# Kernel tuning notes

Hardware: AMD Instinct MI355X
Metric: run time of the kernel (lower is better)

Reference implementation:

```python
import jax, jax.numpy as jnp
import numpy as np

N = 80000          # nodes
E = 1280000        # edges (~avg degree 16)
D_IN = 64          # Lorentz ambient dim (1 time + 63 spatial feature dims)
D_HID = 64
EPS = 1e-8


def _lorentz_inner(x):
    # <x,x>_L = -x0^2 + ||x_space||^2  (keepdims)
    return -x[:, :1] * x[:, :1] + jnp.sum(x[:, 1:] * x[:, 1:], axis=-1, keepdims=True)


def _to_manifold(s):
    # scale so that <s,s>_L = -1 (curvature c=1 hyperboloid)
    denom = jnp.sqrt(jnp.clip(jnp.abs(_lorentz_inner(s)), EPS))
    return s / denom


def _lorentz_linear(x, W, b, log_scale, nonlin=None):
    # HyboNet LorentzLinear: dense map, then rebuild a valid hyperboloid point
    if nonlin is not None:
        x = nonlin(x)
    h = x @ W.T + b
    time = jax.nn.sigmoid(h[:, :1]) * jnp.exp(log_scale) + 1.1
    space = h[:, 1:]
    sq = jnp.clip(jnp.sum(space * space, axis=-1, keepdims=True), EPS)
    scale = (time * time - 1.0) / sq
    return jnp.concatenate([time, space * jnp.sqrt(scale)], axis=-1)


def _agg(h, src, dst, w):
    # sparse adjacency aggregation (spmm) + Lorentz centroid normalization
    s = jax.ops.segment_sum(w[:, None] * h[src], dst, num_segments=N)
    return _to_manifold(s)


def setup_inputs() -> dict:
    key = jax.random.key(0)
    ks = jax.random.split(key, 6)
    x = jax.random.normal(ks[0], (N, D_IN - 1), jnp.float32)
    edge_index = jax.random.randint(ks[1], (2, E), 0, N, dtype=jnp.int32)
    edge_weight = jax.random.uniform(ks[2], (E,), jnp.float32)
    W1 = jax.random.normal(ks[3], (D_HID, D_IN), jnp.float32) * 0.02
    b1 = jnp.zeros((D_HID,), jnp.float32)
    s1 = jnp.asarray(np.log(10.0), jnp.float32)   # LorentzLinear scale param (log-space)
    W2 = jax.random.normal(ks[4], (D_HID, D_HID), jnp.float32) * 0.02
    b2 = jnp.zeros((D_HID,), jnp.float32)
    s2 = jnp.asarray(np.log(10.0), jnp.float32)
    return dict(x=x, edge_index=edge_index, edge_weight=edge_weight,
                W1=W1, b1=b1, s1=s1, W2=W2, b2=b2, s2=s2)


def reference(x, edge_index, edge_weight, W1, b1, s1, W2, b2, s2):
    src, dst = edge_index[0], edge_index[1]
    n = x.shape[0]
    # lift to Lorentz tangent space at origin: prepend zero time coord
    # (proj_tan0 is then a no-op since time component is already 0)
    u_space = x                                             # [N, D_IN-1]
    # expmap0 (c=1): [cosh(||u||), sinh(||u||) * u/||u||]
    nrm = jnp.clip(jnp.linalg.norm(u_space, axis=-1, keepdims=True), EPS)
    p_space = jnp.sinh(nrm) * u_space / nrm
    # projx: recompute time coord from spatial part, x0 = sqrt(1 + ||x_s||^2)
    p_time = jnp.sqrt(1.0 + jnp.sum(p_space * p_space, axis=-1, keepdims=True))
    p = jnp.concatenate([p_time, p_space], axis=1)          # [N, D_IN]
    # conv1 (no nonlin) and conv2 (relu) = LorentzLinear + Lorentz aggregation
    h1 = _agg(_lorentz_linear(p, W1, b1, s1), src, dst, edge_weight)
    h2 = _agg(_lorentz_linear(h1, W2, b2, s2, nonlin=jax.nn.relu), src, dst, edge_weight)
    # LResNet hyperbolic residual: Lorentz-normalized sum of the two points
    return _to_manifold(h1 + h2)
```

## Files before the change

### kernel.cpp

```cpp
#include <hip/hip_runtime.h>
#include <hip/hip_bf16.h>

#define D 64
#define EPS 1e-8f
#define BSH 8
#define BNODES (1 << BSH)
#define ABLK 8192
#define AUNR 32

typedef __attribute__((ext_vector_type(8))) short bf16x8;
typedef __attribute__((ext_vector_type(4))) float f32x4;
typedef unsigned long long ull;

__device__ __forceinline__ unsigned short f2bf_rn(float f) {
    unsigned u = __float_as_uint(f);
    return (unsigned short)((u + 0x7FFFu + ((u >> 16) & 1u)) >> 16);
}

__device__ __forceinline__ void split8(float4 a, float4 b, bf16x8& h, bf16x8& l) {
    float f[8] = {a.x, a.y, a.z, a.w, b.x, b.y, b.z, b.w};
    #pragma unroll
    for (int i = 0; i < 8; ++i) {
        unsigned u = __float_as_uint(f[i]);
        float hf = __uint_as_float(u & 0xFFFF0000u);
        unsigned lu = __float_as_uint(f[i] - hf);
        h[i] = (short)(u >> 16);
        l[i] = (short)(lu >> 16);
    }
}


__device__ __forceinline__ void embed_body(int bid, const float* __restrict__ x,
                                           float* __restrict__ P, int n) {
    int lane = threadIdx.x & 63, wv = threadIdx.x >> 6;
    int q = lane >> 4, sub = lane & 15;
    int node = bid * 16 + wv * 4 + q;
    if (node >= n) return;
    const float* xr = x + (size_t)node * 63;
    float v0 = 0.f, v1, v2, v3;
    if (sub == 0) {
        v1 = xr[0]; v2 = xr[1]; v3 = xr[2];
    } else {
        int b = sub * 4 - 1;
        v0 = xr[b]; v1 = xr[b + 1]; v2 = xr[b + 2]; v3 = xr[b + 3];
    }
    float s = v0 * v0 + v1 * v1 + v2 * v2 + v3 * v3;
    #pragma unroll
    for (int d2 = 1; d2 < 16; d2 <<= 1) s += __shfl_xor(s, d2);
    float nrm = fmaxf(sqrtf(s), EPS);
    float sh = sinhf(nrm);
    float k = sh / nrm;
    float4 r;
    if (sub == 0) r = make_float4(sqrtf(1.f + sh * sh), k * v1, k * v2, k * v3);
    else          r = make_float4(k * v0, k * v1, k * v2, k * v3);
    *(float4*)(P + (size_t)node * 64 + sub * 4) = r;
}

__device__ __forceinline__ void bcount_body(int bid, const int* __restrict__ dst,
                                            int* __restrict__ bcnt, int e, int nbuck) {
    __shared__ int cnt[320];
    int tid = threadIdx.x;
    for (int b = tid; b < nbuck; b += 256) cnt[b] = 0;
    __syncthreads();
    int i0 = bid * 1024 + tid;
    #pragma unroll
    for (int u = 0; u < 4; ++u) {
        int i = i0 + u * 256;
        if (i < e) atomicAdd(&cnt[dst[i] >> BSH], 1);
    }
    __syncthreads();
    for (int b = tid; b < nbuck; b += 256)
        if (cnt[b]) atomicAdd(&bcnt[b], cnt[b]);
}

__device__ __forceinline__ void bucketA_body(int bid, const int* __restrict__ src,
                                             const int* __restrict__ dst,
                                             const float* __restrict__ w,
                                             int* __restrict__ gcur,
                                             ull* __restrict__ tmp,
                                             int e, int nbuck) {
    __shared__ int cnt[320];
    __shared__ int base[320];
    int tid = threadIdx.x;
    for (int b = tid; b < nbuck; b += 256) cnt[b] = 0;
    __syncthreads();
    int i0 = bid * ABLK + tid;
    int bkt[AUNR], rnk[AUNR];
    #pragma unroll
    for (int u = 0; u < AUNR; ++u) {
        int i = i0 + u * 256;
        if (i < e) {
            int b = dst[i] >> BSH;
            bkt[u] = b;
            rnk[u] = atomicAdd(&cnt[b], 1);
        }
    }
    __syncthreads();
    for (int b = tid; b < nbuck; b += 256) {
        int c = cnt[b];
        base[b] = c ? atomicAdd(&gcur[b], c) : 0;
    }
    __syncthreads();
    #pragma unroll
    for (int u = 0; u < AUNR; ++u) {
        int i = i0 + u * 256;
        if (i < e) {
            ull pk = ((ull)__float_as_uint(w[i]) << 32)
                   | (unsigned)(src[i] | ((dst[i] & (BNODES - 1)) << 20));
            tmp[base[bkt[u]] + rnk[u]] = pk;
        }
    }
}

template <int RELU>
__device__ __forceinline__ void lin_body(int bid, const float* __restrict__ tbl,
                                         const float* __restrict__ W,
                                         const float* __restrict__ bias,
                                         const float* __restrict__ sc,
                                         unsigned short* __restrict__ out, int n) {
    int lane = threadIdx.x & 63, wv = threadIdx.x >> 6;
    int col = lane & 15, grp = lane >> 4;
    int node0 = bid * 64 + wv * 16;
    if (node0 >= n) return;

    float es = expf(sc[0]);

    bf16x8 wh[2][4], wl[2][4];
    #pragma unroll
    for (int s = 0; s < 2; ++s)
        #pragma unroll
        for (int t = 0; t < 4; ++t) {
            const float* wp = W + (t * 16 + col) * 64 + s * 32 + grp * 8;
            split8(*(const float4*)wp, *(const float4*)(wp + 4), wh[s][t], wl[s][t]);
        }

    f32x4 acc[4];
    #pragma unroll
    for (int t = 0; t < 4; ++t) {
        float bv = bias[t * 16 + col];
        acc[t] = (f32x4){bv, bv, bv, bv};
    }

    int arow = node0 + col;
    if (arow >= n) arow = n - 1;
    #pragma unroll
    for (int s = 0; s < 2; ++s) {
        const float* ap = tbl + (size_t)arow * 64 + s * 32 + grp * 8;
        float4 a0 = *(const float4*)ap;
        float4 a1 = *(const float4*)(ap + 4);
        if (RELU) {
            a0.x = fmaxf(a0.x, 0.f); a0.y = fmaxf(a0.y, 0.f);
            a0.z = fmaxf(a0.z, 0.f); a0.w = fmaxf(a0.w, 0.f);
            a1.x = fmaxf(a1.x, 0.f); a1.y = fmaxf(a1.y, 0.f);
            a1.z = fmaxf(a1.z, 0.f); a1.w = fmaxf(a1.w, 0.f);
        }
        bf16x8 ah, al;
        split8(a0, a1, ah, al);
        #pragma unroll
        for (int t = 0; t < 4; ++t) {
            acc[t] = __builtin_amdgcn_mfma_f32_16x16x32_bf16(ah, wh[s][t], acc[t], 0, 0, 0);
            acc[t] = __builtin_amdgcn_mfma_f32_16x16x32_bf16(al, wh[s][t], acc[t], 0, 0, 0);
            acc[t] = __builtin_amdgcn_mfma_f32_16x16x32_bf16(ah, wl[s][t], acc[t], 0, 0, 0);
        }
    }

    float tot[4];
    #pragma unroll
    for (int r = 0; r < 4; ++r) {
        float s = 0.f;
        #pragma unroll
        for (int t = 0; t < 4; ++t) s += acc[t][r] * acc[t][r];
        tot[r] = s;
    }
    #pragma unroll
    for (int d2 = 1; d2 < 16; d2 <<= 1) {
        #pragma unroll
        for (int r = 0; r < 4; ++r) tot[r] += __shfl_xor(tot[r], d2);
    }
    float tm[4], rs[4];
    #pragma unroll
    for (int r = 0; r < 4; ++r) {
        float h0 = __shfl(acc[0][r], lane & 48);
        tm[r] = es / (1.f + expf(-h0)) + 1.1f;
        float sq = fmaxf(tot[r] - h0 * h0, EPS);
        rs[r] = sqrtf((tm[r] * tm[r] - 1.f) / sq);
    }
    #pragma unroll
    for (int t = 0; t < 4; ++t) {
        #pragma unroll
        for (int r = 0; r < 4; ++r) {
            int row = node0 + grp * 4 + r;
            if (row < n) {
                int j = t * 16 + col;
                float v = (j == 0) ? tm[r] : acc[t][r] * rs[r];
                out[(size_t)row * 64 + j] = f2bf_rn(v);
            }
        }
    }
}


__global__ __launch_bounds__(256) void k_f1(const float* __restrict__ x,
                                            float* __restrict__ P,
                                            const int* __restrict__ dst,
                                            int* __restrict__ bcnt,
                                            int n, int e, int nbuck, int gEm) {
    if ((int)blockIdx.x < gEm) embed_body(blockIdx.x, x, P, n);
    else                       bcount_body(blockIdx.x - gEm, dst, bcnt, e, nbuck);
}

__global__ __launch_bounds__(512) void k_bscan(const int* __restrict__ bcnt,
                                               int* __restrict__ bstart,
                                               int* __restrict__ gcur,
                                               int* __restrict__ off,
                                               int n, int e, int nbuck) {
    __shared__ int sm[512];
    int tid = threadIdx.x;
    int v = (tid < nbuck) ? bcnt[tid] : 0;
    sm[tid] = v;
    __syncthreads();
    #pragma unroll
    for (int d = 1; d < 512; d <<= 1) {
        int t = (tid >= d) ? sm[tid - d] : 0;
        __syncthreads();
        sm[tid] += t;
        __syncthreads();
    }
    int excl = sm[tid] - v;
    if (tid < nbuck) { bstart[tid] = excl; gcur[tid] = excl; }
    if (tid == 0) { bstart[nbuck] = e; off[n] = e; }
}

__global__ __launch_bounds__(256) void k_f2(const int* __restrict__ src,
                                            const int* __restrict__ dst,
                                            const float* __restrict__ wE,
                                            int* __restrict__ gcur,
                                            ull* __restrict__ tmp,
                                            int e, int nbuck, int nA,
                                            const float* __restrict__ P,
                                            const float* __restrict__ W1,
                                            const float* __restrict__ b1,
                                            const float* __restrict__ s1,
                                            unsigned short* __restrict__ T, int n) {
    if ((int)blockIdx.x < nA) bucketA_body(blockIdx.x, src, dst, wE, gcur, tmp, e, nbuck);
    else                      lin_body<0>(blockIdx.x - nA, P, W1, b1, s1, T, n);
}

__global__ __launch_bounds__(1024) void k_bucketB(const ull* __restrict__ tmp,
                                                  const int* __restrict__ bstart,
                                                  int* __restrict__ off,
                                                  ull* __restrict__ epack,
                                                  int n) {
    __shared__ int cur[BNODES];
    __shared__ int sm[BNODES];
    int b = blockIdx.x;
    int v0 = b << BSH;
    int nv = min(BNODES, n - v0);
    int tid = threadIdx.x;
    if (tid < BNODES) cur[tid] = 0;
    __syncthreads();
    int s0 = bstart[b], s1 = bstart[b + 1];
    for (int i = s0 + tid; i < s1; i += 1024)
        atomicAdd(&cur[((unsigned)tmp[i] >> 20) & (BNODES - 1)], 1);
    __syncthreads();
    int v = 0;
    if (tid < BNODES) { v = cur[tid]; sm[tid] = v; }
    __syncthreads();
    #pragma unroll
    for (int d = 1; d < BNODES; d <<= 1) {
        int t = 0;
        if (tid < BNODES && tid >= d) t = sm[tid - d];
        __syncthreads();
        if (tid < BNODES) sm[tid] += t;
        __syncthreads();
    }
    if (tid < BNODES) {
        int node_off = s0 + sm[tid] - v;
        if (tid < nv) off[v0 + tid] = node_off;
        cur[tid] = node_off;
    }
    __syncthreads();
    for (int i = s0 + tid; i < s1; i += 1024) {
        ull pk = tmp[i];
        int dl = ((unsigned)pk >> 20) & (BNODES - 1);
        int pos = atomicAdd(&cur[dl], 1);
        epack[pos] = pk;
    }
}

__global__ __launch_bounds__(256) void k_lin2(const float* __restrict__ h1,
                                              const float* __restrict__ W2,
                                              const float* __restrict__ b2,
                                              const float* __restrict__ s2,
                                              unsigned short* __restrict__ T, int n) {
    lin_body<1>(blockIdx.x, h1, W2, b2, s2, T, n);
}

template <int FINAL>
__global__ __launch_bounds__(256) void k_agg(const unsigned short* __restrict__ t,
                                             const int* __restrict__ off,
                                             const ull* __restrict__ epack,
                                             const float* __restrict__ h1,
                                             float* __restrict__ out, int n) {
    __shared__ __align__(16) ull ebuf[4][64];
    int lane = threadIdx.x & 63, wv = threadIdx.x >> 6;
    int q = lane >> 4, sub = lane & 15;
    int node = blockIdx.x * 4 + wv;
    if (node >= n) return;
    int s0 = off[node], s1 = off[node + 1];
    float ax = 0.f, ay = 0.f, az = 0.f, aw = 0.f;
    for (int base = s0; base < s1; base += 64) {
        int c = min(s1 - base, 64);
        ull ev = 0;
        if (lane < c) ev = __builtin_nontemporal_load(&epack[base + lane]);
        ebuf[wv][lane] = ev;
        int ng = (c + 3) >> 2;
        uint2 rv[16]; float wgt[16];
        #pragma unroll
        for (int g = 0; g < 16; ++g) {
            if (g < ng) {
                ull e = ebuf[wv][g * 4 + q];
                wgt[g] = __uint_as_float((unsigned)(e >> 32));
                unsigned srcn = (unsigned)e & 0xFFFFFu;
                rv[g] = *(const uint2*)((const unsigned*)(t + ((size_t)srcn << 6)) + sub * 2);
            }
        }
        #pragma unroll
        for (int g = 0; g < 16; ++g) {
            if (g < ng) {
                float w = wgt[g];
                ax += w * __uint_as_float(rv[g].x << 16);
                ay += w * __uint_as_float(rv[g].x & 0xFFFF0000u);
                az += w * __uint_as_float(rv[g].y << 16);
                aw += w * __uint_as_float(rv[g].y & 0xFFFF0000u);
            }
        }
    }
    #pragma unroll
    for (int d2 = 16; d2 <= 32; d2 <<= 1) {
        ax += __shfl_xor(ax, d2);
        ay += __shfl_xor(ay, d2);
        az += __shfl_xor(az, d2);
        aw += __shfl_xor(aw, d2);
    }
    float s = ay * ay + az * az + aw * aw;
    s += (sub == 0) ? -ax * ax : ax * ax;
    #pragma unroll
    for (int d2 = 1; d2 < 16; d2 <<= 1) s += __shfl_xor(s, d2);
    float inv = 1.f / sqrtf(fmaxf(fabsf(s), EPS));
    float hx = ax * inv, hy = ay * inv, hz = az * inv, hw = aw * inv;
    if (FINAL) {
        f32x4 hv = __builtin_nontemporal_load(
            (const f32x4*)(h1 + (size_t)node * 64 + sub * 4));
        float vx = hv[0] + hx, vy = hv[1] + hy, vz = hv[2] + hz, vw = hv[3] + hw;
        float s2 = vy * vy + vz * vz + vw * vw;
        s2 += (sub == 0) ? -vx * vx : vx * vx;
        #pragma unroll
        for (int d2 = 1; d2 < 16; d2 <<= 1) s2 += __shfl_xor(s2, d2);
        float inv2 = 1.f / sqrtf(fmaxf(fabsf(s2), EPS));
        if (lane < 16) {
            float4 r = make_float4(vx * inv2, vy * inv2, vz * inv2, vw * inv2);
            *(float4*)(out + (size_t)node * 64 + sub * 4) = r;
        }
    } else {
        if (lane < 16) {
            float4 r = make_float4(hx, hy, hz, hw);
            *(float4*)(out + (size_t)node * 64 + sub * 4) = r;
        }
    }
}

extern "C" void kernel_launch(void* const* d_in, const int* in_sizes, int n_in,
                              void* d_out, int out_size, void* d_ws, size_t ws_size,
                              hipStream_t stream) {
    const float* x  = (const float*)d_in[0];
    const int*   ei = (const int*)d_in[1];
    const float* wE = (const float*)d_in[2];
    const float* W1 = (const float*)d_in[3];
    const float* b1 = (const float*)d_in[4];
    const float* s1 = (const float*)d_in[5];
    const float* W2 = (const float*)d_in[6];
    const float* b2 = (const float*)d_in[7];
    const float* s2 = (const float*)d_in[8];
    float* out = (float*)d_out;

    const int N = in_sizes[0] / (D - 1);
    const int E = in_sizes[2];
    const int* src = ei;
    const int* dst = ei + E;
    const int nbuck = (N + BNODES - 1) >> BSH;

    char* ws = (char*)d_ws;
    unsigned short* T = (unsigned short*)ws;
    float* B2 = (float*)(ws + (((size_t)N * D * 2 + 255) & ~(size_t)255));
    ull* epack = (ull*)((char*)B2 + (size_t)N * D * 4);
    ull* tmp   = epack + E;
    int* off    = (int*)(tmp + E);
    int* bcnt   = off + (N + 1);
    int* bstart = bcnt + 320;
    int* gcur   = bstart + 320;

    hipMemsetAsync(bcnt, 0, 320 * sizeof(int), stream);

    int gE4 = (E + 1023) / 1024;
    int gEm = (N + 15) / 16;
    int nA  = (E + ABLK - 1) / ABLK;
    int gL  = (N + 63) / 64;
    int gA  = (N + 3) / 4;

    k_f1<<<gEm + gE4, 256, 0, stream>>>(x, B2, dst, bcnt, N, E, nbuck, gEm);
    k_bscan<<<1, 512, 0, stream>>>(bcnt, bstart, gcur, off, N, E, nbuck);
    k_f2<<<nA + gL, 256, 0, stream>>>(src, dst, wE, gcur, tmp, E, nbuck, nA,
                                      B2, W1, b1, s1, T, N);
    k_bucketB<<<nbuck, 1024, 0, stream>>>(tmp, bstart, off, epack, N);

    k_agg<0><<<gA, 256, 0, stream>>>(T, off, epack, nullptr, B2, N);
    k_lin2<<<gL, 256, 0, stream>>>(B2, W2, b2, s2, T, N);
    k_agg<1><<<gA, 256, 0, stream>>>(T, off, epack, B2, out, N);
}
```

Before: 198.3 us.

## Locally sort edges by bucket in shared memory before coalesced scatter

The bucket scatter pass now does a full block-local counting sort. It counts per bucket, runs a wave-level prefix scan for local offsets, and places edge indices into a shared-memory array ordered by bucket. Each wave then writes a bucket's edges contiguously to the global temp buffer, replacing scattered per-edge 8-byte stores with mostly coalesced runs. The cost is a second shared atomic pass, 32 KB of shared memory (which may lower occupancy), extra syncs, and gathered re-reads of src/dst/w.

```diff
diff --git a/kernel.cpp b/kernel.cpp
--- a/kernel.cpp
+++ b/kernel.cpp
@@ -79,35 +79,69 @@
                                              int* __restrict__ gcur,
                                              ull* __restrict__ tmp,
                                              int e, int nbuck) {
+    __shared__ unsigned sidx[ABLK];
     __shared__ int cnt[320];
-    __shared__ int base[320];
+    __shared__ int lbase[324];
+    __shared__ int gbase[320];
     int tid = threadIdx.x;
+    int i0 = bid * ABLK;
     for (int b = tid; b < nbuck; b += 256) cnt[b] = 0;
     __syncthreads();
-    int i0 = bid * ABLK + tid;
-    int bkt[AUNR], rnk[AUNR];
     #pragma unroll
     for (int u = 0; u < AUNR; ++u) {
-        int i = i0 + u * 256;
-        if (i < e) {
-            int b = dst[i] >> BSH;
-            bkt[u] = b;
-            rnk[u] = atomicAdd(&cnt[b], 1);
-        }
+        int i = i0 + u * 256 + tid;
+        if (i < e) atomicAdd(&cnt[dst[i] >> BSH], 1);
+    }
+    __syncthreads();
+    if (tid < 64) {
+        int b5 = tid * 5;
+        int loc[5]; int s = 0;
+        #pragma unroll
+        for (int k = 0; k < 5; ++k) {
+            int b = b5 + k;
+            loc[k] = s;
+            s += (b < nbuck) ? cnt[b] : 0;
+        }
+        int incl = s;
+        #pragma unroll
+        for (int d2 = 1; d2 < 64; d2 <<= 1) {
+            int t = __shfl_up(incl, d2);
+            if (tid >= d2) incl += t;
+        }
+        int excl = incl - s;
+        #pragma unroll
+        for (int k = 0; k < 5; ++k) {
+            int b = b5 + k;
+            if (b < nbuck) lbase[b] = excl + loc[k];
+        }
+        if (tid == 63) lbase[nbuck] = incl;
     }
     __syncthreads();
     for (int b = tid; b < nbuck; b += 256) {
         int c = cnt[b];
-        base[b] = c ? atomicAdd(&gcur[b], c) : 0;
+        gbase[b] = c ? atomicAdd(&gcur[b], c) : 0;
+        cnt[b] = lbase[b];
     }
     __syncthreads();
     #pragma unroll
     for (int u = 0; u < AUNR; ++u) {
-        int i = i0 + u * 256;
+        int i = i0 + u * 256 + tid;
         if (i < e) {
+            int slot = atomicAdd(&cnt[dst[i] >> BSH], 1);
+            sidx[slot] = (unsigned)i;
+        }
+    }
+    __syncthreads();
+    int wv = tid >> 6, lane = tid & 63;
+    for (int b = wv; b < nbuck; b += 4) {
+        int lb = lbase[b];
+        int len = lbase[b + 1] - lb;
+        int gb = gbase[b];
+        for (int j = lane; j < len; j += 64) {
+            int i = (int)sidx[lb + j];
             ull pk = ((ull)__float_as_uint(w[i]) << 32)
                    | (unsigned)(src[i] | ((dst[i] & (BNODES - 1)) << 20));
-            tmp[base[bkt[u]] + rnk[u]] = pk;
+            tmp[gb + j] = pk;
         }
     }
 }
```

Measured after the change: 215.3 us. +8.6%, slower.

## Fuse first aggregation with second Lorentz linear and interleave embed/bucket-count blocks

Applied to the files above, without the earlier changes.

Merges the layer-1 aggregation kernel with the layer-2 LorentzLinear (MFMA bf16 split-precision matmul) so that each block aggregates 16 nodes, stages the ReLU'd rows in shared memory and applies W2 directly. This drops one launch and the reload of h1 for the matmul. T1 and T2 now sit in separate buffers to avoid a race. In exchange, the aggregation loop is no longer unrolled and only one wave does the matmul while the others sit idle. Separately, the first kernel interleaves bucket-count blocks with embed blocks across the grid instead of placing them at the end, to balance the load.

```diff
diff --git a/kernel.cpp b/kernel.cpp
--- a/kernel.cpp
+++ b/kernel.cpp
@@ -204,9 +204,14 @@
                                             float* __restrict__ P,
                                             const int* __restrict__ dst,
                                             int* __restrict__ bcnt,
-                                            int n, int e, int nbuck, int gEm) {
-    if ((int)blockIdx.x < gEm) embed_body(blockIdx.x, x, P, n);
-    else                       bcount_body(blockIdx.x - gEm, dst, bcnt, e, nbuck);
+                                            int n, int e, int nbuck,
+                                            int gEm, int gB) {
+    int bid = blockIdx.x;
+    int total = gEm + gB;
+    int a = (int)(((long long)bid * gB) / total);
+    int b = (int)(((long long)(bid + 1) * gB) / total);
+    if (b > a) bcount_body(a, dst, bcnt, e, nbuck);
+    else       embed_body(bid - a, x, P, n);
 }
 
 __global__ __launch_bounds__(512) void k_bscan(const int* __restrict__ bcnt,
@@ -288,20 +293,145 @@
     }
 }
 
-__global__ __launch_bounds__(256) void k_lin2(const float* __restrict__ h1,
-                                              const float* __restrict__ W2,
-                                              const float* __restrict__ b2,
-                                              const float* __restrict__ s2,
-                                              unsigned short* __restrict__ T, int n) {
-    lin_body<1>(blockIdx.x, h1, W2, b2, s2, T, n);
-}
-
-template <int FINAL>
-__global__ __launch_bounds__(256) void k_agg(const unsigned short* __restrict__ t,
-                                             const int* __restrict__ off,
-                                             const ull* __restrict__ epack,
-                                             const float* __restrict__ h1,
-                                             float* __restrict__ out, int n) {
+__global__ __launch_bounds__(256, 6) void k_aggF(const unsigned short* __restrict__ t,
+                                                 const int* __restrict__ off,
+                                                 const ull* __restrict__ epack,
+                                                 const float* __restrict__ W2,
+                                                 const float* __restrict__ b2,
+                                                 const float* __restrict__ s2,
+                                                 float* __restrict__ h1,
+                                                 unsigned short* __restrict__ T2,
+                                                 int n) {
+    __shared__ __align__(16) ull ebuf[4][64];
+    __shared__ float hbuf[16][65];
+    int tid = threadIdx.x;
+    int lane = tid & 63, wv = tid >> 6;
+    int q = lane >> 4, sub = lane & 15;
+    int nb0 = blockIdx.x * 16;
+
+    #pragma unroll 1
+    for (int k = 0; k < 4; ++k) {
+        int node = nb0 + wv * 4 + k;
+        int ln = wv * 4 + k;
+        float hx = 0.f, hy = 0.f, hz = 0.f, hw = 0.f;
+        if (node < n) {
+            int s0 = off[node], s1 = off[node + 1];
+            float ax = 0.f, ay = 0.f, az = 0.f, aw = 0.f;
+            for (int base = s0; base < s1; base += 64) {
+                int c = min(s1 - base, 64);
+                ull ev = 0;
+                if (lane < c) ev = __builtin_nontemporal_load(&epack[base + lane]);
+                ebuf[wv][lane] = ev;
+                int c4 = (c + 3) & ~3;
+                for (int j = 0; j < c4; j += 4) {
+                    ull e = ebuf[wv][j + q];
+                    float w = __uint_as_float((unsigned)(e >> 32));
+                    unsigned srcn = (unsigned)e & 0xFFFFFu;
+                    uint2 rv = *(const uint2*)((const unsigned*)(t + ((size_t)srcn << 6)) + sub * 2);
+                    ax += w * __uint_as_float(rv.x << 16);
+                    ay += w * __uint_as_float(rv.x & 0xFFFF0000u);
+                    az += w * __uint_as_float(rv.y << 16);
+                    aw += w * __uint_as_float(rv.y & 0xFFFF0000u);
+                }
+            }
+            #pragma unroll
+            for (int d2 = 16; d2 <= 32; d2 <<= 1) {
+                ax += __shfl_xor(ax, d2);
+                ay += __shfl_xor(ay, d2);
+                az += __shfl_xor(az, d2);
+                aw += __shfl_xor(aw, d2);
+            }
+            float s = ay * ay + az * az + aw * aw;
+            s += (sub == 0) ? -ax * ax : ax * ax;
+            #pragma unroll
+            for (int d2 = 1; d2 < 16; d2 <<= 1) s += __shfl_xor(s, d2);
+            float inv = 1.f / sqrtf(fmaxf(fabsf(s), EPS));
+            hx = ax * inv; hy = ay * inv; hz = az * inv; hw = aw * inv;
+            if (lane < 16)
+                *(float4*)(h1 + (size_t)node * 64 + sub * 4) = make_float4(hx, hy, hz, hw);
+        }
+        if (lane < 16) {
+            hbuf[ln][sub * 4 + 0] = fmaxf(hx, 0.f);
+            hbuf[ln][sub * 4 + 1] = fmaxf(hy, 0.f);
+            hbuf[ln][sub * 4 + 2] = fmaxf(hz, 0.f);
+            hbuf[ln][sub * 4 + 3] = fmaxf(hw, 0.f);
+        }
+    }
+    __syncthreads();
+
+    if (wv == 0 && nb0 < n) {
+        int col = lane & 15, grp = lane >> 4;
+        float es = expf(s2[0]);
+        bf16x8 wh[2][4], wl[2][4];
+        #pragma unroll
+        for (int s = 0; s < 2; ++s)
+            #pragma unroll
+            for (int tt = 0; tt < 4; ++tt) {
+                const float* wp = W2 + (tt * 16 + col) * 64 + s * 32 + grp * 8;
+                split8(*(const float4*)wp, *(const float4*)(wp + 4), wh[s][tt], wl[s][tt]);
+            }
+        f32x4 accd[4];
+        #pragma unroll
+        for (int tt = 0; tt < 4; ++tt) {
+            float bv = b2[tt * 16 + col];
+            accd[tt] = (f32x4){bv, bv, bv, bv};
+        }
+        #pragma unroll
+        for (int s = 0; s < 2; ++s) {
+            float a8[8];
+            #pragma unroll
+            for (int j = 0; j < 8; ++j) a8[j] = hbuf[col][s * 32 + grp * 8 + j];
+            bf16x8 ah, al;
+            split8(make_float4(a8[0], a8[1], a8[2], a8[3]),
+                   make_float4(a8[4], a8[5], a8[6], a8[7]), ah, al);
+            #pragma unroll
+            for (int tt = 0; tt < 4; ++tt) {
+                accd[tt] = __builtin_amdgcn_mfma_f32_16x16x32_bf16(ah, wh[s][tt], accd[tt], 0, 0, 0);
+                accd[tt] = __builtin_amdgcn_mfma_f32_16x16x32_bf16(al, wh[s][tt], accd[tt], 0, 0, 0);
+                accd[tt] = __builtin_amdgcn_mfma_f32_16x16x32_bf16(ah, wl[s][tt], accd[tt], 0, 0, 0);
+            }
+        }
+        float tot[4];
+        #pragma unroll
+        for (int r = 0; r < 4; ++r) {
+            float s = 0.f;
+            #pragma unroll
+            for (int tt = 0; tt < 4; ++tt) s += accd[tt][r] * accd[tt][r];
+            tot[r] = s;
+        }
+        #pragma unroll
+        for (int d2 = 1; d2 < 16; d2 <<= 1) {
+            #pragma unroll
+            for (int r = 0; r < 4; ++r) tot[r] += __shfl_xor(tot[r], d2);
+        }
+        float tm[4], rs[4];
+        #pragma unroll
+        for (int r = 0; r < 4; ++r) {
+            float h0 = __shfl(accd[0][r], lane & 48);
+            tm[r] = es / (1.f + expf(-h0)) + 1.1f;
+            float sq = fmaxf(tot[r] - h0 * h0, EPS);
+            rs[r] = sqrtf((tm[r] * tm[r] - 1.f) / sq);
+        }
+        #pragma unroll
+        for (int tt = 0; tt < 4; ++tt) {
+            #pragma unroll
+            for (int r = 0; r < 4; ++r) {
+                int row = nb0 + grp * 4 + r;
+                if (row < n) {
+                    int j = tt * 16 + col;
+                    float v = (j == 0) ? tm[r] : accd[tt][r] * rs[r];
+                    T2[(size_t)row * 64 + j] = f2bf_rn(v);
+                }
+            }
+        }
+    }
+}
+
+__global__ __launch_bounds__(256) void k_agg2(const unsigned short* __restrict__ t,
+                                              const int* __restrict__ off,
+                                              const ull* __restrict__ epack,
+                                              const float* __restrict__ h1,
+                                              float* __restrict__ out, int n) {
     __shared__ __align__(16) ull ebuf[4][64];
     int lane = threadIdx.x & 63, wv = threadIdx.x >> 6;
     int q = lane >> 4, sub = lane & 15;
@@ -349,24 +479,17 @@
     for (int d2 = 1; d2 < 16; d2 <<= 1) s += __shfl_xor(s, d2);
     float inv = 1.f / sqrtf(fmaxf(fabsf(s), EPS));
     float hx = ax * inv, hy = ay * inv, hz = az * inv, hw = aw * inv;
-    if (FINAL) {
-        f32x4 hv = __builtin_nontemporal_load(
-            (const f32x4*)(h1 + (size_t)node * 64 + sub * 4));
-        float vx = hv[0] + hx, vy = hv[1] + hy, vz = hv[2] + hz, vw = hv[3] + hw;
-        float s2 = vy * vy + vz * vz + vw * vw;
-        s2 += (sub == 0) ? -vx * vx : vx * vx;
-        #pragma unroll
-        for (int d2 = 1; d2 < 16; d2 <<= 1) s2 += __shfl_xor(s2, d2);
-        float inv2 = 1.f / sqrtf(fmaxf(fabsf(s2), EPS));
-        if (lane < 16) {
-            float4 r = make_float4(vx * inv2, vy * inv2, vz * inv2, vw * inv2);
-            *(float4*)(out + (size_t)node * 64 + sub * 4) = r;
-        }
-    } else {
-        if (lane < 16) {
-            float4 r = make_float4(hx, hy, hz, hw);
-            *(float4*)(out + (size_t)node * 64 + sub * 4) = r;
-        }
+    f32x4 hv = __builtin_nontemporal_load(
+        (const f32x4*)(h1 + (size_t)node * 64 + sub * 4));
+    float vx = hv[0] + hx, vy = hv[1] + hy, vz = hv[2] + hz, vw = hv[3] + hw;
+    float s2 = vy * vy + vz * vz + vw * vw;
+    s2 += (sub == 0) ? -vx * vx : vx * vx;
+    #pragma unroll
+    for (int d2 = 1; d2 < 16; d2 <<= 1) s2 += __shfl_xor(s2, d2);
+    float inv2 = 1.f / sqrtf(fmaxf(fabsf(s2), EPS));
+    if (lane < 16) {
+        float4 r = make_float4(vx * inv2, vy * inv2, vz * inv2, vw * inv2);
+        *(float4*)(out + (size_t)node * 64 + sub * 4) = r;
     }
 }
 
@@ -391,8 +514,10 @@
     const int nbuck = (N + BNODES - 1) >> BSH;
 
     char* ws = (char*)d_ws;
-    unsigned short* T = (unsigned short*)ws;
-    float* B2 = (float*)(ws + (((size_t)N * D * 2 + 255) & ~(size_t)255));
+    size_t szT = (((size_t)N * D * 2) + 255) & ~(size_t)255;
+    unsigned short* T1 = (unsigned short*)ws;
+    unsigned short* T2 = (unsigned short*)(ws + szT);
+    float* B2 = (float*)(ws + 2 * szT);
     ull* epack = (ull*)((char*)B2 + (size_t)N * D * 4);
     ull* tmp   = epack + E;
     int* off    = (int*)(tmp + E);
@@ -406,15 +531,15 @@
     int gEm = (N + 15) / 16;
     int nA  = (E + ABLK - 1) / ABLK;
     int gL  = (N + 63) / 64;
-    int gA  = (N + 3) / 4;
-
-    k_f1<<<gEm + gE4, 256, 0, stream>>>(x, B2, dst, bcnt, N, E, nbuck, gEm);
+    int gAF = (N + 15) / 16;
+    int gA2 = (N + 3) / 4;
+
+    k_f1<<<gEm + gE4, 256, 0, stream>>>(x, B2, dst, bcnt, N, E, nbuck, gEm, gE4);
     k_bscan<<<1, 512, 0, stream>>>(bcnt, bstart, gcur, off, N, E, nbuck);
     k_f2<<<nA + gL, 256, 0, stream>>>(src, dst, wE, gcur, tmp, E, nbuck, nA,
-                                      B2, W1, b1, s1, T, N);
+                                      B2, W1, b1, s1, T1, N);
     k_bucketB<<<nbuck, 1024, 0, stream>>>(tmp, bstart, off, epack, N);
 
-    k_agg<0><<<gA, 256, 0, stream>>>(T, off, epack, nullptr, B2, N);
-    k_lin2<<<gL, 256, 0, stream>>>(B2, W2, b2, s2, T, N);
-    k_agg<1><<<gA, 256, 0, stream>>>(T, off, epack, B2, out, N);
-}
+    k_aggF<<<gAF, 256, 0, stream>>>(T1, off, epack, W2, b2, s2, B2, T2, N);
+    k_agg2<<<gA2, 256, 0, stream>>>(T2, off, epack, B2, out, N);
+}
```

Result: slower. 206.5 us (+4.1%).
